# Optimization experiments

Hardware: AMD Instinct MI355X
Metric: run time of the kernel (lower is better)

The kernel has to match this reference:

```python
import jax, jax.numpy as jnp
from jax import lax
import numpy as np

B = 128   # per-stream batch (hard-coded via torch.zeros(128, ...))
T = 224   # timesteps
L = 224   # per-timestep signal length
H = 12    # LSTM hidden size


def _conv_chain(x, w1, b1, w2, b2):
    # x: [N, 1, 224] -> [N, 1, 28]
    # Conv1d(k=8, s=4, p=2) -> ReLU -> MaxPool1d(k=4, s=2, p=1) -> ReLU -> Conv1d(k=3, s=1, p=1) -> ReLU
    y = lax.conv_general_dilated(x, w1, (4,), [(2, 2)]) + b1[None, :, None]          # [N,1,56]
    y = jax.nn.relu(y)
    y = lax.reduce_window(y, -jnp.inf, lax.max, (1, 1, 4), (1, 1, 2),
                          [(0, 0), (0, 0), (1, 1)])                                   # [N,1,28]
    y = jax.nn.relu(y)
    y = lax.conv_general_dilated(y, w2, (1,), [(1, 1)]) + b2[None, :, None]          # [N,1,28]
    return jax.nn.relu(y)


def _lstm_bidir(x, Wih, Whh, b):
    # x: [B, T, D]; Wih: [2, 4H, D]; Whh: [2, 4H, H]; b: [2, 4H]; gates in PyTorch order i,f,g,o
    Bn, hid = x.shape[0], Whh.shape[-1]

    def run(xs, wih, whh, bb):
        def step(carry, xt):
            h, c = carry
            g = xt @ wih.T + h @ whh.T + bb
            i, f, gg, o = jnp.split(g, 4, axis=-1)
            c = jax.nn.sigmoid(f) * c + jax.nn.sigmoid(i) * jnp.tanh(gg)
            h = jax.nn.sigmoid(o) * jnp.tanh(c)
            return (h, c), h
        h0 = jnp.zeros((Bn, hid), x.dtype)
        _, ys = lax.scan(step, (h0, h0), xs)
        return ys

    xs = jnp.swapaxes(x, 0, 1)                     # [T, B, D]
    fwd = run(xs, Wih[0], Whh[0], b[0])
    bwd = run(xs[::-1], Whh_fix := Wih[1], Whh[1], b[1])[::-1]
    return jnp.swapaxes(jnp.concatenate([fwd, bwd], axis=-1), 0, 1)  # [B, T, 2H]


def _forward(x, c1w1, c1b1, c1w2, c1b2, c2w1, c2b1, c2w2, c2b2,
             l1_0_Wih, l1_0_Whh, l1_0_b, l1_1_Wih, l1_1_Whh, l1_1_b,
             l2_0_Wih, l2_0_Whh, l2_0_b, l2_1_Wih, l2_1_Whh, l2_1_b,
             fcw1, fcb1, fcw2, fcb2, fcw3, fcb3, w1, w2):
    x1 = x[:B, 0]          # [B, 224, 224]
    x2 = x[B:2 * B, 0]     # [B, 224, 224]
    # Fuse the 224-step Python loop: fold time into the batch of the 1D conv.
    y1 = _conv_chain(x1.reshape(B * T, 1, L), c1w1, c1b1, c1w2, c1b2).reshape(B, T, 28)
    y2 = _conv_chain(x2.reshape(B * T, 1, L), c2w1, c2b1, c2w2, c2b2).reshape(B, T, 28)
    o1 = _lstm_bidir(_lstm_bidir(y1, l1_0_Wih, l1_0_Whh, l1_0_b), l1_1_Wih, l1_1_Whh, l1_1_b)
    o2 = _lstm_bidir(_lstm_bidir(y2, l2_0_Wih, l2_0_Whh, l2_0_b), l2_1_Wih, l2_1_Whh, l2_1_b)
    out = w1 * o1 + w2 * o2                       # [B, T, 24]
    out = out.reshape(B, T * 2 * H)               # [B, 5376]
    out = out @ fcw1.T + fcb1                     # [B, 1024]
    out = out @ fcw2.T + fcb2                     # [B, 192]
    return out @ fcw3.T + fcb3                    # [B, 9]


def setup_inputs():
    key = jax.random.key(0)
    ks = iter(jax.random.split(key, 48))

    def rn(shape, scale=0.1):
        return (scale * jax.random.normal(next(ks), shape)).astype(jnp.float32)

    inp = {"x": rn((2 * B, 1, T, L), 1.0)}
    for s in ("c1", "c2"):
        inp[s + "w1"] = rn((1, 1, 8))
        inp[s + "b1"] = rn((1,))
        inp[s + "w2"] = rn((1, 1, 3))
        inp[s + "b2"] = rn((1,))
    for s in ("l1", "l2"):
        for layer, din in ((0, 28), (1, 2 * H)):
            inp[f"{s}_{layer}_Wih"] = rn((2, 4 * H, din))
            inp[f"{s}_{layer}_Whh"] = rn((2, 4 * H, H))
            inp[f"{s}_{layer}_b"] = rn((2, 4 * H))
    inp["fcw1"] = rn((1024, T * 2 * H), 0.02)
    inp["fcb1"] = rn((1024,))
    inp["fcw2"] = rn((192, 1024), 0.05)
    inp["fcb2"] = rn((192,))
    inp["fcw3"] = rn((9, 192), 0.05)
    inp["fcb3"] = rn((9,))
    inp["w1"] = jnp.ones((1,), jnp.float32)
    inp["w2"] = jnp.ones((1,), jnp.float32)
    return inp


def reference(x, c1w1, c1b1, c1w2, c1b2, c2w1, c2b1, c2w2, c2b2,
              l1_0_Wih, l1_0_Whh, l1_0_b, l1_1_Wih, l1_1_Whh, l1_1_b,
              l2_0_Wih, l2_0_Whh, l2_0_b, l2_1_Wih, l2_1_Whh, l2_1_b,
              fcw1, fcb1, fcw2, fcb2, fcw3, fcb3, w1, w2):
    return _forward(x, c1w1, c1b1, c1w2, c1b2, c2w1, c2b1, c2w2, c2b2,
                    l1_0_Wih, l1_0_Whh, l1_0_b, l1_1_Wih, l1_1_Whh, l1_1_b,
                    l2_0_Wih, l2_0_Whh, l2_0_b, l2_1_Wih, l2_1_Whh, l2_1_b,
                    fcw1, fcb1, fcw2, fcb2, fcw3, fcb3, w1, w2)
```

## Files before the change

### kernel.cpp

```cpp
#include <hip/hip_runtime.h>

#define BB 128
#define TT 224
#define LL 224

typedef float v2f __attribute__((ext_vector_type(2)));

__device__ __forceinline__ float rcpf(float x){ return __builtin_amdgcn_rcpf(x); }

#if __has_builtin(__builtin_amdgcn_exp2f)
#define EXP2(x) __builtin_amdgcn_exp2f(x)
#else
#define EXP2(x) __expf((x)*0.6931471805599453f)
#endif

template<int N>
__device__ __forceinline__ float rorN(float x){
  int xi = __builtin_bit_cast(int, x);
  xi = __builtin_amdgcn_update_dpp(xi, xi, 0x120 + N, 0xf, 0xf, false);
  return __builtin_bit_cast(float, xi);
}

__device__ __forceinline__ void swap32(float& a, float& b){
  asm volatile("s_nop 1\n\tv_permlane32_swap_b32 %0, %1\n\ts_nop 1"
               : "+v"(a), "+v"(b));
}

#define LSTM_STEP(P, SS) { \
  float x1=rorN<1>(hv), x2=rorN<2>(hv), x3=rorN<3>(hv), x4=rorN<4>(hv), \
        x5=rorN<5>(hv), x6=rorN<6>(hv), x7=rorN<7>(hv), x8=rorN<8>(hv), \
        x9=rorN<9>(hv), x10=rorN<10>(hv), x11=rorN<11>(hv), x12=rorN<12>(hv), \
        x13=rorN<13>(hv), x14=rorN<14>(hv), x15=rorN<15>(hv); \
  v2f a0 = (P); \
  a0 += w[0]*(v2f){hv,hv};   a0 += w[1]*(v2f){x1,x1};   a0 += w[2]*(v2f){x2,x2};   a0 += w[3]*(v2f){x3,x3}; \
  v2f a1 = w[4]*(v2f){x4,x4};   a1 += w[5]*(v2f){x5,x5};   a1 += w[6]*(v2f){x6,x6};   a1 += w[7]*(v2f){x7,x7}; \
  v2f a2 = w[8]*(v2f){x8,x8};   a2 += w[9]*(v2f){x9,x9};   a2 += w[10]*(v2f){x10,x10}; a2 += w[11]*(v2f){x11,x11}; \
  v2f a3 = w[12]*(v2f){x12,x12}; a3 += w[13]*(v2f){x13,x13}; a3 += w[14]*(v2f){x14,x14}; a3 += w[15]*(v2f){x15,x15}; \
  v2f gg = (a0+a1)+(a2+a3); \
  v2f m  = gg*kmul; \
  v2f e  = { EXP2(m.x), EXP2(m.y) }; \
  e += (v2f){1.f,1.f}; \
  v2f d  = { rcpf(e.x), rcpf(e.y) }; \
  v2f res = ca*d + cb; \
  float p0 = res.x, p1 = res.x; swap32(p0, p1); \
  float q0 = res.y, q1 = res.y; swap32(q0, q1); \
  cst = fmaf(q0, cst, p0*p1); \
  float et = EXP2(cst*2.885390082f); \
  float dt = rcpf(et+1.f); \
  hv = q1*fmaf(-2.f, dt, 1.f); \
  hbuf[SS] = hv; }

#define FLUSH8 { \
  if (doSt){ \
    _Pragma("unroll") \
    for (int q=0;q<8;q++) outP[q*ostep] = hbuf[q]; \
  } \
  outP += 8*ostep; }

#define LSTM_PREP(WHH) \
  v2f w[16]; \
  _Pragma("unroll") \
  for (int rr=0; rr<16; rr++){ \
    int j = (u - rr) & 15; \
    bool vld = (j < 12) && (u < 12); \
    int uw = (u < 12) ? u : 0; \
    int jw = (j < 12) ? j : 0; \
    float wa = (WHH)[((rbit?24:0)  + uw)*12 + jw]; \
    float wb = (WHH)[((rbit?36:12) + uw)*12 + jw]; \
    w[rr] = (v2f){ vld ? wa : 0.f, vld ? wb : 0.f }; \
  } \
  const v2f kmul = rbit ? (v2f){2.885390082f, -1.442695041f} \
                        : (v2f){-1.442695041f, -1.442695041f}; \
  const v2f ca   = rbit ? (v2f){-2.f, 1.f} : (v2f){1.f, 1.f}; \
  const v2f cb   = rbit ? (v2f){ 1.f, 0.f} : (v2f){0.f, 0.f};

#define LSTM_CONSUME3(LPRE, OUTBUF) { \
  float* preR = (LPRE) + bh*(224*48) + keff*4 + rbit*2; \
  const int sstep = dir ? -48 : 48; \
  int scb = dir ? 223*48 : 0; \
  volatile int* pv = prog; \
  while (pv[0] < 2 || pv[1] < 2 || pv[2] < 2) __builtin_amdgcn_s_sleep(2); \
  asm volatile("" ::: "memory"); \
  v2f pcur[8], pnext[8]; \
  _Pragma("unroll") \
  for (int i=0;i<8;i++) pcur[i]  = *(const v2f*)(preR + scb +  i   *sstep); \
  _Pragma("unroll") \
  for (int i=0;i<8;i++) pnext[i] = *(const v2f*)(preR + scb + (i+8)*sstep); \
  int lb = scb + 16*sstep; \
  float hv = 0.f, cst = 0.f; \
  float hbuf[8]; \
  const int ostep = dir ? -24 : 24; \
  float* outP = (OUTBUF) + (size_t)br*(BB*TT*24) + (size_t)b*TT*24 + dir*12 + u \
              + (size_t)(dir ? 223 : 0)*24; \
  const bool doSt = (rbit==0) && (u < 12); \
  for (int c=0;c<14;c++){ \
    LSTM_STEP(pcur[0],0) LSTM_STEP(pcur[1],1) LSTM_STEP(pcur[2],2) LSTM_STEP(pcur[3],3) \
    LSTM_STEP(pcur[4],4) LSTM_STEP(pcur[5],5) LSTM_STEP(pcur[6],6) LSTM_STEP(pcur[7],7) \
    FLUSH8 \
    if (c < 13){ \
      int nd_ = 2*c+3; \
      while (pv[0] < nd_ || pv[1] < nd_ || pv[2] < nd_) __builtin_amdgcn_s_sleep(2); \
      asm volatile("" ::: "memory"); \
      _Pragma("unroll") \
      for (int i=0;i<8;i++) pcur[i] = *(const v2f*)(preR + lb + i*sstep); \
      lb += 8*sstep; \
    } \
    LSTM_STEP(pnext[0],0) LSTM_STEP(pnext[1],1) LSTM_STEP(pnext[2],2) LSTM_STEP(pnext[3],3) \
    LSTM_STEP(pnext[4],4) LSTM_STEP(pnext[5],5) LSTM_STEP(pnext[6],6) LSTM_STEP(pnext[7],7) \
    FLUSH8 \
    if (c < 13){ \
      int nd_ = 2*c+4; \
      while (pv[0] < nd_ || pv[1] < nd_ || pv[2] < nd_) __builtin_amdgcn_s_sleep(2); \
      asm volatile("" ::: "memory"); \
      _Pragma("unroll") \
      for (int i=0;i<8;i++) pnext[i] = *(const v2f*)(preR + lb + i*sstep); \
      lb += 8*sstep; \
    } \
  } }

__global__ __launch_bounds__(256) void wtb_kernel(
    const float* __restrict__ fcw2, const float* __restrict__ fcw3,
    float* __restrict__ Wtb)
{
  int idx = blockIdx.x*256 + threadIdx.x;
  int o = idx >> 10, n = idx & 1023;
  float acc = 0.f;
  for (int p=0;p<192;p++) acc += fcw3[o*192+p]*fcw2[(size_t)p*1024+n];
  Wtb[idx] = acc;
}

__global__ __launch_bounds__(256) __attribute__((amdgpu_waves_per_eu(1,1)))
void lstm1_fused_kernel(const float* __restrict__ x,
    const float* __restrict__ whhA, const float* __restrict__ whhB,
    const float* __restrict__ wihA, const float* __restrict__ biasA,
    const float* __restrict__ wihB, const float* __restrict__ biasB,
    const float* __restrict__ c1w1, const float* __restrict__ c1b1,
    const float* __restrict__ c1w2, const float* __restrict__ c1b2,
    const float* __restrict__ c2w1, const float* __restrict__ c2b1,
    const float* __restrict__ c2w2, const float* __restrict__ c2b2,
    const float* __restrict__ fcw1, const float* __restrict__ fcb1,
    const float* __restrict__ Wtb,
    float* __restrict__ wpart, float* __restrict__ BCpart,
    float* __restrict__ out)
{
  __shared__ float lpre[2*224*48];
  __shared__ float ybuf[2*224*28];
  __shared__ float c1s[16*57];
  __shared__ float wtscr[3*576];
  __shared__ int prog[8];
  int tid  = threadIdx.x;
  int blk  = blockIdx.x;
  int r    = blk >> 6;
  int br   = r >> 1, dir = r & 1;
  int b0   = (blk & 63)*2;

  if (tid < 8) ((volatile int*)prog)[tid] = 0;
  __syncthreads();

  if (tid >= 64){
    if (tid < 128){
      int p    = tid - 64;
      int rowq = p >> 2;
      int q    = p & 3;
      int bb   = rowq >> 3;
      int ti   = rowq & 7;
      int cjs  = q*14;
      const float* w1 = br ? c2w1 : c1w1;
      const float* w2 = br ? c2w2 : c1w2;
      float b1  = br ? c2b1[0] : c1b1[0];
      float b2v = br ? c2b2[0] : c1b2[0];
      float w1r[8];
      #pragma unroll
      for (int kk=0;kk<8;kk++) w1r[kk]=w1[kk];
      float w2r[3];
      #pragma unroll
      for (int kk=0;kk<3;kk++) w2r[kk]=w2[kk];
      const float* xb = x + ((size_t)(br*128 + b0 + bb))*50176;
      volatile int* pv = prog;
      int a0 = 4*cjs - 4;

      for (int g=0; g<28; ++g){
        int step = g*8 + ti;
        int t = dir ? 223-step : step;
        const float* xrow = xb + (size_t)t*224;
        float xr[64];
        #pragma unroll
        for (int qq=0; qq<16; qq++){
          int idx = a0 + 4*qq;
          if (idx >= 0 && idx <= 220){
            float4 v = *(const float4*)(xrow + idx);
            xr[4*qq]=v.x; xr[4*qq+1]=v.y; xr[4*qq+2]=v.z; xr[4*qq+3]=v.w;
          } else {
            #pragma unroll
            for (int e=0;e<4;e++){
              int ii = idx+e;
              xr[4*qq+e] = (ii>=0 && ii<224) ? xrow[ii] : 0.f;
            }
          }
        }
        #pragma unroll
        for (int e=0;e<14;e++){
          float s = b1;
          #pragma unroll
          for (int kk=0;kk<8;kk++) s += xr[4*e+2+kk]*w1r[kk];
          c1s[rowq*57 + cjs + e] = fmaxf(s, 0.f);
        }
        asm volatile("s_waitcnt lgkmcnt(0)" ::: "memory");
        const float* cr = &c1s[rowq*57];
        #pragma unroll
        for (int jj=0;jj<7;jj++){
          int j = q*7 + jj;
          float o = b2v;
          #pragma unroll
          for (int pi=0;pi<3;pi++){
            int pp = j - 1 + pi;
            float pool = 0.f;
            if (pp>=0 && pp<28){
              int i0 = 2*pp - 1;
              float m = -1e30f;
              #pragma unroll
              for (int q2=0;q2<4;q2++){
                int ii = i0+q2;
                if (ii>=0 && ii<56) m = fmaxf(m, cr[ii]);
              }
              pool = fmaxf(m, 0.f);
            }
            o += pool * w2r[pi];
          }
          ybuf[(bb*224 + t)*28 + j] = fmaxf(o, 0.f);
        }
        asm volatile("s_waitcnt lgkmcnt(0)" ::: "memory");
        if (p == 0) pv[0] = g+1;
      }
    } else {
      int p2 = tid - 128;
      if (p2 < 96){
        int fidx = (tid >> 6) - 1;
        int bb   = p2 / 48;
        int gate = p2 % 48;
        const float* wih2 = (br ? wihB : wihA) + (dir*48 + gate)*28;
        float4 wq[7];
        #pragma unroll
        for (int q=0;q<7;q++) wq[q] = ((const float4*)wih2)[q];
        float bias = (br ? biasB : biasA)[dir*48 + gate];
        int unit = gate % 12, gg = gate / 12;
        float* lrow = lpre + bb*(224*48) + unit*4 + gg;
        volatile int* pv = prog;

        for (int g=0; g<28; ++g){
          while (pv[0] < g+1) __builtin_amdgcn_s_sleep(2);
          asm volatile("" ::: "memory");
          #pragma unroll
          for (int si=0; si<8; si++){
            int t = dir ? 223-(g*8+si) : (g*8+si);
            const float4* yr = (const float4*)&ybuf[(bb*224 + t)*28];
            float a = bias;
            #pragma unroll
            for (int q=0;q<7;q++){
              float4 yq = yr[q];
              a += yq.x*wq[q].x + yq.y*wq[q].y + yq.z*wq[q].z + yq.w*wq[q].w;
            }
            lrow[t*48] = a;
          }
          asm volatile("s_waitcnt lgkmcnt(0)" ::: "memory");
          if ((p2 & 63) == 0) pv[fidx] = g+1;
        }
      }
    }

    {
      int wv   = (tid >> 6) - 1;
      int lane = tid & 63;
      float* wt = wtscr + wv*576;
      for (int tk = blk*3 + wv; tk < 1344; tk += 768){
        int s = tk / 84, j64 = tk % 84;
        #pragma unroll
        for (int q=0;q<9;q++) wt[q*64+lane] = Wtb[q*1024 + s*64 + lane];
        asm volatile("s_waitcnt lgkmcnt(0) vmcnt(0)" ::: "memory");
        int j = j64*64 + lane;
        int nbase = s*64;
        float acc[9];
        #pragma unroll
        for (int o=0;o<9;o++) acc[o]=0.f;
        #pragma unroll 4
        for (int n4=0;n4<16;n4++){
          int nb = nbase + n4*4;
          float4 v4;
          v4.x = fcw1[(size_t)(nb  )*5376 + j];
          v4.y = fcw1[(size_t)(nb+1)*5376 + j];
          v4.z = fcw1[(size_t)(nb+2)*5376 + j];
          v4.w = fcw1[(size_t)(nb+3)*5376 + j];
          #pragma unroll
          for (int o=0;o<9;o++){
            float4 w4 = *(const float4*)&wt[o*64 + n4*4];
            acc[o] += v4.x*w4.x + v4.y*w4.y + v4.z*w4.z + v4.w*w4.w;
          }
        }
        #pragma unroll
        for (int o=0;o<9;o++) wpart[((size_t)s*9+o)*5376 + j] = acc[o];
        if (j64 == 0 && lane < 9){
          float bcp = 0.f;
          for (int n=0;n<64;n++) bcp += wt[lane*64+n]*fcb1[nbase+n];
          BCpart[s*9+lane] = bcp;
        }
        asm volatile("s_waitcnt lgkmcnt(0)" ::: "memory");
      }
    }
    return;
  }

  int lane = tid;
  int u    = lane & 15;
  int bh   = (lane >> 4) & 1;
  int rbit = lane >> 5;
  int keff = (u < 12) ? u : 11;
  int b    = b0 + bh;
  const float* whh = (br ? whhB : whhA) + dir*48*12;
  LSTM_PREP(whh)
  LSTM_CONSUME3(lpre, out)
}

__global__ __launch_bounds__(256) __attribute__((amdgpu_waves_per_eu(1,1)))
void lstm2_fused_kernel(const float* __restrict__ ol0,
    const float* __restrict__ whhA, const float* __restrict__ whhB,
    const float* __restrict__ wihA, const float* __restrict__ biasA,
    const float* __restrict__ wihB, const float* __restrict__ biasB,
    const float* __restrict__ wpart, float* __restrict__ Wc,
    const float* __restrict__ fcw3, const float* __restrict__ fcb2,
    const float* __restrict__ fcb3, const float* __restrict__ BCpart,
    float* __restrict__ BC,
    float* __restrict__ out)
{
  __shared__ float lpre[2*224*48];
  __shared__ int prog[8];
  int tid  = threadIdx.x;
  int blk  = blockIdx.x;
  int r    = blk >> 6;
  int br   = r >> 1, dir = r & 1;
  int b0   = (blk & 63)*2;

  if (tid < 8) ((volatile int*)prog)[tid] = 0;
  __syncthreads();

  if (tid >= 64){
    int p    = tid - 64;
    int wv   = p >> 6;
    int e    = p % 96;
    int th   = p / 96;
    int bb   = e / 48;
    int gate = e % 48;
    const float* wih2 = (br ? wihB : wihA) + (dir*48 + gate)*24;
    float4 wq[6];
    #pragma unroll
    for (int q=0;q<6;q++) wq[q] = ((const float4*)wih2)[q];
    float bias = (br ? biasB : biasA)[dir*48 + gate];
    int unit = gate % 12, gg = gate / 12;
    const float* olrow = ol0 + (size_t)br*(BB*TT*24) + (size_t)(b0+bb)*TT*24;
    float* lrow = lpre + bb*(224*48) + unit*4 + gg;
    volatile int* pv = prog;

    for (int g=0; g<28; g++){
      #pragma unroll
      for (int si=0; si<4; si++){
        int step = g*8 + th*4 + si;
        int t = dir ? 223 - step : step;
        const float4* xr = (const float4*)(olrow + t*24);
        float a = bias;
        #pragma unroll
        for (int q=0;q<6;q++){
          float4 xq = xr[q];
          a += xq.x*wq[q].x + xq.y*wq[q].y + xq.z*wq[q].z + xq.w*wq[q].w;
        }
        lrow[t*48] = a;
      }
      asm volatile("s_waitcnt lgkmcnt(0) vmcnt(0)" ::: "memory");
      if ((p & 63) == 0) pv[wv] = g+1;
    }

    {
      int lane = p & 63;
      int tk = blk*3 + wv;
      if (tk < 756){
        int idx = tk*64 + lane;
        float a = 0.f;
        #pragma unroll
        for (int s=0;s<16;s++) a += wpart[(size_t)s*48384 + idx];
        Wc[idx] = a;
      }
      if (blk == 255 && wv == 2 && lane < 9){
        float acc = fcb3[lane];
        const float* f3 = fcw3 + lane*192;
        for (int pp=0;pp<192;pp++) acc += f3[pp]*fcb2[pp];
        #pragma unroll
        for (int s=0;s<16;s++) acc += BCpart[s*9+lane];
        BC[lane] = acc;
      }
    }
    return;
  }

  int lane = tid;
  int u    = lane & 15;
  int bh   = (lane >> 4) & 1;
  int rbit = lane >> 5;
  int keff = (u < 12) ? u : 11;
  int b    = b0 + bh;
  const float* whh = (br ? whhB : whhA) + dir*48*12;
  LSTM_PREP(whh)
  LSTM_CONSUME3(lpre, out)
}

__global__ void final_kernel(const float* __restrict__ o1, const float* __restrict__ o2,
    const float* __restrict__ Wc, const float* __restrict__ BC,
    const float* __restrict__ w1p, const float* __restrict__ w2p,
    float* __restrict__ out)
{
  int wid  = blockIdx.x*4 + (threadIdx.x>>6);
  int lane = threadIdx.x & 63;
  if (wid >= 128*9) return;
  int m = wid / 9, o = wid - m*9;
  float w1 = w1p[0], w2 = w2p[0];
  const float* r1 = o1 + (size_t)m*5376;
  const float* r2 = o2 + (size_t)m*5376;
  const float* wc = Wc + (size_t)o*5376;
  float acc = 0.f;
  for (int i=lane;i<5376;i+=64){
    acc += (w1*r1[i] + w2*r2[i]) * wc[i];
  }
  #pragma unroll
  for (int off=32;off;off>>=1) acc += __shfl_down(acc, off);
  if (lane==0) out[m*9+o] = acc + BC[o];
}

extern "C" void kernel_launch(void* const* d_in, const int* in_sizes, int n_in,
                              void* d_out, int out_size, void* d_ws, size_t ws_size,
                              hipStream_t stream) {
  (void)in_sizes; (void)n_in; (void)out_size; (void)ws_size;
  const float* x    = (const float*)d_in[0];
  const float* c1w1 = (const float*)d_in[1];
  const float* c1b1 = (const float*)d_in[2];
  const float* c1w2 = (const float*)d_in[3];
  const float* c1b2 = (const float*)d_in[4];
  const float* c2w1 = (const float*)d_in[5];
  const float* c2b1 = (const float*)d_in[6];
  const float* c2w2 = (const float*)d_in[7];
  const float* c2b2 = (const float*)d_in[8];
  const float* l10Wih = (const float*)d_in[9];
  const float* l10Whh = (const float*)d_in[10];
  const float* l10b   = (const float*)d_in[11];
  const float* l11Wih = (const float*)d_in[12];
  const float* l11Whh = (const float*)d_in[13];
  const float* l11b   = (const float*)d_in[14];
  const float* l20Wih = (const float*)d_in[15];
  const float* l20Whh = (const float*)d_in[16];
  const float* l20b   = (const float*)d_in[17];
  const float* l21Wih = (const float*)d_in[18];
  const float* l21Whh = (const float*)d_in[19];
  const float* l21b   = (const float*)d_in[20];
  const float* fcw1 = (const float*)d_in[21];
  const float* fcb1 = (const float*)d_in[22];
  const float* fcw2 = (const float*)d_in[23];
  const float* fcb2 = (const float*)d_in[24];
  const float* fcw3 = (const float*)d_in[25];
  const float* fcb3 = (const float*)d_in[26];
  const float* w1   = (const float*)d_in[27];
  const float* w2   = (const float*)d_in[28];
  float* out = (float*)d_out;

  float* ws  = (float*)d_ws;
  float* wpart = ws;
  float* ol0  = ws + 2*802816 + 4*1376256;
  float* ol1  = ol0 + 2*688128;
  float* Wc   = ol1 + 2*688128;
  float* BC   = Wc  + 48384;
  float* BCpart = BC + 9;
  float* Wtb  = BCpart + 144;

  wtb_kernel<<<36,256,0,stream>>>(fcw2, fcw3, Wtb);
  lstm1_fused_kernel<<<256,256,0,stream>>>(x, l10Whh, l20Whh,
      l10Wih, l10b, l20Wih, l20b,
      c1w1,c1b1,c1w2,c1b2, c2w1,c2b1,c2w2,c2b2,
      fcw1, fcb1, Wtb, wpart, BCpart, ol0);
  lstm2_fused_kernel<<<256,256,0,stream>>>(ol0, l11Whh, l21Whh,
      l11Wih, l11b, l21Wih, l21b,
      wpart, Wc, fcw3, fcb2, fcb3, BCpart, BC, ol1);
  final_kernel<<<288,256,0,stream>>>(ol1, ol1+688128, Wc, BC, w1, w2, out);
}
```

Measured before the change: 152.4 us.

## Rebalance conv and input-projection wave roles, pad ybuf row stride

The conv producer stage now runs on two waves, one per batch row, with 8 lanes per timestep instead of 4. The input-projection stage shrinks to a single wave, where some lanes compute two gate rows. Each conv wave publishes its own progress flag, and the projection waits on both. The ybuf row stride is padded from 28 to 36 floats to reduce LDS bank conflicts. The aim is to stop the conv stage from starving the pipeline, at the cost of more serial work per projection lane and a more complex flag protocol.

```diff
diff --git a/kernel.cpp b/kernel.cpp
--- a/kernel.cpp
+++ b/kernel.cpp
@@ -144,7 +144,7 @@
     float* __restrict__ out)
 {
   __shared__ float lpre[2*224*48];
-  __shared__ float ybuf[2*224*28];
+  __shared__ float ybuf[2*224*36];
   __shared__ float c1s[16*57];
   __shared__ float wtscr[3*576];
   __shared__ int prog[8];
@@ -158,13 +158,13 @@
   __syncthreads();
 
   if (tid >= 64){
-    if (tid < 128){
-      int p    = tid - 64;
-      int rowq = p >> 2;
-      int q    = p & 3;
-      int bb   = rowq >> 3;
-      int ti   = rowq & 7;
-      int cjs  = q*14;
+    if (tid < 192){
+      int bb = (tid >> 6) - 1;
+      int p  = tid & 63;
+      int ti = p >> 3;
+      int q  = p & 7;
+      int cj0 = q*7;
+      int rowq = bb*8 + ti;
       const float* w1 = br ? c2w1 : c1w1;
       const float* w2 = br ? c2w2 : c1w2;
       float b1  = br ? c2b1[0] : c1b1[0];
@@ -177,15 +177,15 @@
       for (int kk=0;kk<3;kk++) w2r[kk]=w2[kk];
       const float* xb = x + ((size_t)(br*128 + b0 + bb))*50176;
       volatile int* pv = prog;
-      int a0 = 4*cjs - 4;
+      int a0 = 4*cj0 - 4;
 
       for (int g=0; g<28; ++g){
         int step = g*8 + ti;
         int t = dir ? 223-step : step;
         const float* xrow = xb + (size_t)t*224;
-        float xr[64];
-        #pragma unroll
-        for (int qq=0; qq<16; qq++){
+        float xr[40];
+        #pragma unroll
+        for (int qq=0; qq<10; qq++){
           int idx = a0 + 4*qq;
           if (idx >= 0 && idx <= 220){
             float4 v = *(const float4*)(xrow + idx);
@@ -199,72 +199,98 @@
           }
         }
         #pragma unroll
-        for (int e=0;e<14;e++){
+        for (int e=0;e<7;e++){
           float s = b1;
           #pragma unroll
           for (int kk=0;kk<8;kk++) s += xr[4*e+2+kk]*w1r[kk];
-          c1s[rowq*57 + cjs + e] = fmaxf(s, 0.f);
+          c1s[rowq*57 + cj0 + e] = fmaxf(s, 0.f);
         }
         asm volatile("s_waitcnt lgkmcnt(0)" ::: "memory");
-        const float* cr = &c1s[rowq*57];
-        #pragma unroll
-        for (int jj=0;jj<7;jj++){
-          int j = q*7 + jj;
-          float o = b2v;
+        if (q < 4){
+          const float* cr = &c1s[rowq*57];
           #pragma unroll
-          for (int pi=0;pi<3;pi++){
-            int pp = j - 1 + pi;
-            float pool = 0.f;
-            if (pp>=0 && pp<28){
-              int i0 = 2*pp - 1;
-              float m = -1e30f;
-              #pragma unroll
-              for (int q2=0;q2<4;q2++){
-                int ii = i0+q2;
-                if (ii>=0 && ii<56) m = fmaxf(m, cr[ii]);
+          for (int jj=0;jj<7;jj++){
+            int j = q*7 + jj;
+            float o = b2v;
+            #pragma unroll
+            for (int pi=0;pi<3;pi++){
+              int pp = j - 1 + pi;
+              float pool = 0.f;
+              if (pp>=0 && pp<28){
+                int i0 = 2*pp - 1;
+                float m = -1e30f;
+                #pragma unroll
+                for (int q2=0;q2<4;q2++){
+                  int ii = i0+q2;
+                  if (ii>=0 && ii<56) m = fmaxf(m, cr[ii]);
+                }
+                pool = fmaxf(m, 0.f);
               }
-              pool = fmaxf(m, 0.f);
+              o += pool * w2r[pi];
             }
-            o += pool * w2r[pi];
+            ybuf[(bb*224 + t)*36 + j] = fmaxf(o, 0.f);
           }
-          ybuf[(bb*224 + t)*28 + j] = fmaxf(o, 0.f);
         }
         asm volatile("s_waitcnt lgkmcnt(0)" ::: "memory");
-        if (p == 0) pv[0] = g+1;
+        if (p == 0) pv[bb] = g+1;
       }
     } else {
-      int p2 = tid - 128;
-      if (p2 < 96){
-        int fidx = (tid >> 6) - 1;
-        int bb   = p2 / 48;
-        int gate = p2 % 48;
-        const float* wih2 = (br ? wihB : wihA) + (dir*48 + gate)*28;
-        float4 wq[7];
-        #pragma unroll
-        for (int q=0;q<7;q++) wq[q] = ((const float4*)wih2)[q];
-        float bias = (br ? biasB : biasA)[dir*48 + gate];
-        int unit = gate % 12, gg = gate / 12;
-        float* lrow = lpre + bb*(224*48) + unit*4 + gg;
-        volatile int* pv = prog;
-
-        for (int g=0; g<28; ++g){
-          while (pv[0] < g+1) __builtin_amdgcn_s_sleep(2);
-          asm volatile("" ::: "memory");
-          #pragma unroll
-          for (int si=0; si<8; si++){
-            int t = dir ? 223-(g*8+si) : (g*8+si);
-            const float4* yr = (const float4*)&ybuf[(bb*224 + t)*28];
-            float a = bias;
+      int p3 = tid - 192;
+      int bb1   = p3 / 48;
+      int gate1 = p3 % 48;
+      const float* wihA2 = (br ? wihB : wihA);
+      const float* biaA2 = (br ? biasB : biasA);
+      const float* wp1 = wihA2 + (dir*48 + gate1)*28;
+      float4 wq1[7];
+      #pragma unroll
+      for (int q=0;q<7;q++) wq1[q] = ((const float4*)wp1)[q];
+      float bias1 = biaA2[dir*48 + gate1];
+      int unit1 = gate1 % 12, gg1 = gate1 / 12;
+      float* lrow1 = lpre + bb1*(224*48) + unit1*4 + gg1;
+      bool has2 = (p3 < 32);
+      int gate2 = 16 + p3;
+      float4 wq2[7];
+      float bias2 = 0.f;
+      float* lrow2 = lpre;
+      if (has2){
+        const float* wp2 = wihA2 + (dir*48 + gate2)*28;
+        #pragma unroll
+        for (int q=0;q<7;q++) wq2[q] = ((const float4*)wp2)[q];
+        bias2 = biaA2[dir*48 + gate2];
+        int unit2 = gate2 % 12, gg2 = gate2 / 12;
+        lrow2 = lpre + 1*(224*48) + unit2*4 + gg2;
+      }
+      volatile int* pv = prog;
+
+      for (int g=0; g<28; ++g){
+        while (pv[0] < g+1 || pv[1] < g+1) __builtin_amdgcn_s_sleep(2);
+        asm volatile("" ::: "memory");
+        #pragma unroll
+        for (int si=0; si<8; si++){
+          int t = dir ? 223-(g*8+si) : (g*8+si);
+          {
+            const float4* yr = (const float4*)&ybuf[(bb1*224 + t)*36];
+            float a = bias1;
             #pragma unroll
             for (int q=0;q<7;q++){
               float4 yq = yr[q];
-              a += yq.x*wq[q].x + yq.y*wq[q].y + yq.z*wq[q].z + yq.w*wq[q].w;
+              a += yq.x*wq1[q].x + yq.y*wq1[q].y + yq.z*wq1[q].z + yq.w*wq1[q].w;
             }
-            lrow[t*48] = a;
+            lrow1[t*48] = a;
           }
-          asm volatile("s_waitcnt lgkmcnt(0)" ::: "memory");
-          if ((p2 & 63) == 0) pv[fidx] = g+1;
-        }
+          if (has2){
+            const float4* yr = (const float4*)&ybuf[(224 + t)*36];
+            float a = bias2;
+            #pragma unroll
+            for (int q=0;q<7;q++){
+              float4 yq = yr[q];
+              a += yq.x*wq2[q].x + yq.y*wq2[q].y + yq.z*wq2[q].z + yq.w*wq2[q].w;
+            }
+            lrow2[t*48] = a;
+          }
+        }
+        asm volatile("s_waitcnt lgkmcnt(0)" ::: "memory");
+        if (p3 == 0) pv[2] = g+1;
       }
     }
 
```

Result: slower. 195.1 us (+28.1%).
